# Kernel tuning notes

Measured on AMD Instinct MI355X. Metric: run time of the kernel, lower is better.

Reference implementation:

```python
import jax, jax.numpy as jnp
import numpy as np

PAD = 0

def setup_inputs() -> dict:
    key = jax.random.key(0)
    k1, k2, k3, k4 = jax.random.split(key, 4)
    B, S, F, V, H, D = 64, 256, 4, 50257, 768, 512
    words = jax.random.randint(k1, (B, S, F), 0, V, dtype=jnp.int64)  # pad_index=0 occurs rarely at random
    E = jax.random.normal(k2, (V, H), dtype=jnp.float32) * 0.02      # stand-in for transformer last_hidden_state producer
    W = jax.random.normal(k3, (H, D), dtype=jnp.float32) * 0.02      # FFN projection weight
    b = jax.random.normal(k4, (D,), dtype=jnp.float32) * 0.02
    return {"words": words, "E": E, "W": W, "b": b}

def reference(words, E, W, b):
    # words: [B, S, F] subword ids; mask out pad subwords
    mask = (words != PAD)                                  # [B,S,F] bool
    sub = E[words] * mask[..., None].astype(E.dtype)       # [B,S,F,H], pads zeroed
    cnt = mask.sum(-1).astype(E.dtype)                     # [B,S] subwords per word
    # segment-mean over the fix_len axis; fully-padded words -> 0 (matches pad_sequence(..., 0))
    word_emb = sub.sum(-2) / jnp.maximum(cnt, 1.0)[..., None]   # [B,S,H]
    word_emb = jnp.where((cnt > 0)[..., None], word_emb, 0.0)
    return word_emb @ W + b                                # [B,S,D]
```

## Files before the change

### kernel.cpp

```cpp
#include <hip/hip_runtime.h>
#include <hip/hip_bf16.h>

#define M_TOT 16384
#define K_TOT 768
#define N_TOT 512

typedef __attribute__((ext_vector_type(8))) __bf16 bf16x8;
typedef __attribute__((ext_vector_type(4))) float f32x4;

static __device__ __forceinline__ ushort f2bf(float x) {
  union { float f; unsigned int u; } v; v.f = x;
  unsigned int r = v.u + 0x7fffu + ((v.u >> 16) & 1u);
  return (ushort)(r >> 16);
}

static __device__ __forceinline__ void load_lds16(const ushort* g, ushort* l) {
  __builtin_amdgcn_global_load_lds(
      (const __attribute__((address_space(1))) void*)g,
      (__attribute__((address_space(3))) void*)l, 16, 0, 0);
}

__global__ __launch_bounds__(256) void prep_kernel(
    const int* __restrict__ words, const float* __restrict__ E,
    const float* __restrict__ W, ushort* __restrict__ A,
    ushort* __restrict__ Wt) {
  const int bid = blockIdx.x;
  const int t = threadIdx.x;
  if (bid < M_TOT / 4) {
    const int row  = bid * 4 + (t >> 6);
    const int lane = t & 63;
    const int4 w4 = *reinterpret_cast<const int4*>(words + (size_t)row * 4);
    const int ids[4] = {w4.x, w4.y, w4.z, w4.w};

    float a[12];
#pragma unroll
    for (int i = 0; i < 12; ++i) a[i] = 0.f;
    float cnt = 0.f;

#pragma unroll
    for (int f = 0; f < 4; ++f) {
      const int id = ids[f];
      if (id != 0) {
        const float4* __restrict__ src =
            reinterpret_cast<const float4*>(E + (size_t)id * K_TOT);
#pragma unroll
        for (int c = 0; c < 3; ++c) {
          const float4 v = src[c * 64 + lane];
          a[c * 4 + 0] += v.x; a[c * 4 + 1] += v.y;
          a[c * 4 + 2] += v.z; a[c * 4 + 3] += v.w;
        }
        cnt += 1.f;
      }
    }
    const float s = (cnt > 0.f) ? (1.f / cnt) : 0.f;
    ushort* dst = A + (size_t)row * K_TOT;
#pragma unroll
    for (int c = 0; c < 3; ++c) {
      ushort4 o;
      o.x = f2bf(a[c * 4 + 0] * s);
      o.y = f2bf(a[c * 4 + 1] * s);
      o.z = f2bf(a[c * 4 + 2] * s);
      o.w = f2bf(a[c * 4 + 3] * s);
      *reinterpret_cast<ushort4*>(dst + c * 256 + lane * 4) = o;
    }
  } else {
    __shared__ float tile[64][65];
    const int b2 = bid - M_TOT / 4;
    const int k0 = (b2 % (K_TOT / 64)) * 64;
    const int n0 = (b2 / (K_TOT / 64)) * 64;
#pragma unroll
    for (int i = 0; i < 4; ++i) {
      const int idx = t + i * 256;
      const int r = idx >> 4;
      const int c = (idx & 15) * 4;
      const float4 v = *reinterpret_cast<const float4*>(
          W + (size_t)(k0 + r) * N_TOT + n0 + c);
      tile[r][c + 0] = v.x; tile[r][c + 1] = v.y;
      tile[r][c + 2] = v.z; tile[r][c + 3] = v.w;
    }
    __syncthreads();
#pragma unroll
    for (int i = 0; i < 4; ++i) {
      const int idx = t + i * 256;
      const int rn = idx >> 4;
      const int ck = (idx & 15) * 4;
      ushort4 o;
      o.x = f2bf(tile[ck + 0][rn]);
      o.y = f2bf(tile[ck + 1][rn]);
      o.z = f2bf(tile[ck + 2][rn]);
      o.w = f2bf(tile[ck + 3][rn]);
      *reinterpret_cast<ushort4*>(Wt + (size_t)(n0 + rn) * K_TOT + k0 + ck) = o;
    }
  }
}

__global__ __launch_bounds__(256) void gemm_kernel(
    const ushort* __restrict__ A, const ushort* __restrict__ Bt,
    const float* __restrict__ bias, float* __restrict__ out) {
  __shared__ ushort Al[128 * 64];
  __shared__ ushort Bl[128 * 64];
  const int t    = threadIdx.x;
  const int lane = t & 63;
  const int w    = t >> 6;
  const int bm   = blockIdx.x >> 2;
  const int bn   = blockIdx.x & 3;
  const int wr   = w >> 1;
  const int wc   = w & 1;

  f32x4 acc[4][4];
#pragma unroll
  for (int m = 0; m < 4; ++m)
#pragma unroll
    for (int n = 0; n < 4; ++n) acc[m][n] = (f32x4){0.f, 0.f, 0.f, 0.f};

  const int srow = t >> 3;
  const int sseg = t & 7;
  const ushort* aptr = A  + (size_t)(bm * 128 + srow) * K_TOT + sseg * 8;
  const ushort* bptr = Bt + (size_t)(bn * 128 + srow) * K_TOT + sseg * 8;

  for (int kt = 0; kt < K_TOT / 64; ++kt) {
    __syncthreads();
#pragma unroll
    for (int i = 0; i < 4; ++i) {
      load_lds16(aptr + (size_t)i * 32 * K_TOT + kt * 64,
                 &Al[(i * 256 + w * 64) * 8]);
      load_lds16(bptr + (size_t)i * 32 * K_TOT + kt * 64,
                 &Bl[(i * 256 + w * 64) * 8]);
    }
    __syncthreads();

#pragma unroll
    for (int kk = 0; kk < 2; ++kk) {
      bf16x8 af[4], bf_[4];
      const int ks = kk * 4 + (lane >> 4);
#pragma unroll
      for (int m = 0; m < 4; ++m)
        af[m] = *reinterpret_cast<const bf16x8*>(
            &Al[(wr * 64 + m * 16 + (lane & 15)) * 64 + ks * 8]);
#pragma unroll
      for (int n = 0; n < 4; ++n)
        bf_[n] = *reinterpret_cast<const bf16x8*>(
            &Bl[(wc * 64 + n * 16 + (lane & 15)) * 64 + ks * 8]);
#pragma unroll
      for (int m = 0; m < 4; ++m)
#pragma unroll
        for (int n = 0; n < 4; ++n)
          acc[m][n] = __builtin_amdgcn_mfma_f32_16x16x32_bf16(
              af[m], bf_[n], acc[m][n], 0, 0, 0);
    }
  }

  const int colBase = bn * 128 + wc * 64 + (lane & 15);
  const int rowBase = bm * 128 + wr * 64 + ((lane >> 4) << 2);
#pragma unroll
  for (int n = 0; n < 4; ++n) {
    const float bv = bias[colBase + n * 16];
#pragma unroll
    for (int m = 0; m < 4; ++m) {
#pragma unroll
      for (int j = 0; j < 4; ++j) {
        out[(size_t)(rowBase + m * 16 + j) * N_TOT + colBase + n * 16] =
            acc[m][n][j] + bv;
      }
    }
  }
}

extern "C" void kernel_launch(void* const* d_in, const int* in_sizes, int n_in,
                              void* d_out, int out_size, void* d_ws,
                              size_t ws_size, hipStream_t stream) {
  const int*   words = (const int*)d_in[0];
  const float* E     = (const float*)d_in[1];
  const float* W     = (const float*)d_in[2];
  const float* b     = (const float*)d_in[3];
  float* out = (float*)d_out;

  ushort* Aws  = (ushort*)d_ws;
  ushort* Wtws = Aws + (size_t)M_TOT * K_TOT;

  hipLaunchKernelGGL(prep_kernel,
                     dim3(M_TOT / 4 + (K_TOT / 64) * (N_TOT / 64)), dim3(256),
                     0, stream, words, E, W, Aws, Wtws);
  hipLaunchKernelGGL(gemm_kernel, dim3((M_TOT / 128) * (N_TOT / 128)),
                     dim3(256), 0, stream, Aws, Wtws, b, out);
}
```

Baseline: 62.49 us.

## Double-buffer GEMM LDS tiles, branchless gather masking, nontemporal output stores

```diff
diff --git a/kernel.cpp b/kernel.cpp
--- a/kernel.cpp
+++ b/kernel.cpp
@@ -40,16 +40,15 @@
 #pragma unroll
     for (int f = 0; f < 4; ++f) {
       const int id = ids[f];
-      if (id != 0) {
-        const float4* __restrict__ src =
-            reinterpret_cast<const float4*>(E + (size_t)id * K_TOT);
-#pragma unroll
-        for (int c = 0; c < 3; ++c) {
-          const float4 v = src[c * 64 + lane];
-          a[c * 4 + 0] += v.x; a[c * 4 + 1] += v.y;
-          a[c * 4 + 2] += v.z; a[c * 4 + 3] += v.w;
-        }
-        cnt += 1.f;
+      const float msk = (id != 0) ? 1.f : 0.f;
+      cnt += msk;
+      const float4* __restrict__ src =
+          reinterpret_cast<const float4*>(E + (size_t)id * K_TOT);
+#pragma unroll
+      for (int c = 0; c < 3; ++c) {
+        const float4 v = src[c * 64 + lane];
+        a[c * 4 + 0] += v.x * msk; a[c * 4 + 1] += v.y * msk;
+        a[c * 4 + 2] += v.z * msk; a[c * 4 + 3] += v.w * msk;
       }
     }
     const float s = (cnt > 0.f) ? (1.f / cnt) : 0.f;
@@ -97,8 +96,8 @@
 __global__ __launch_bounds__(256) void gemm_kernel(
     const ushort* __restrict__ A, const ushort* __restrict__ Bt,
     const float* __restrict__ bias, float* __restrict__ out) {
-  __shared__ ushort Al[128 * 64];
-  __shared__ ushort Bl[128 * 64];
+  __shared__ ushort Al[2][128 * 64];
+  __shared__ ushort Bl[2][128 * 64];
   const int t    = threadIdx.x;
   const int lane = t & 63;
   const int w    = t >> 6;
@@ -118,37 +117,52 @@
   const ushort* aptr = A  + (size_t)(bm * 128 + srow) * K_TOT + sseg * 8;
   const ushort* bptr = Bt + (size_t)(bn * 128 + srow) * K_TOT + sseg * 8;
 
-  for (int kt = 0; kt < K_TOT / 64; ++kt) {
-    __syncthreads();
-#pragma unroll
-    for (int i = 0; i < 4; ++i) {
-      load_lds16(aptr + (size_t)i * 32 * K_TOT + kt * 64,
-                 &Al[(i * 256 + w * 64) * 8]);
-      load_lds16(bptr + (size_t)i * 32 * K_TOT + kt * 64,
-                 &Bl[(i * 256 + w * 64) * 8]);
-    }
-    __syncthreads();
-
+#define STAGE(buf, kt)                                                       \
+  do {                                                                       \
+    _Pragma("unroll") for (int i = 0; i < 4; ++i) {                          \
+      load_lds16(aptr + (size_t)i * 32 * K_TOT + (kt) * 64,                  \
+                 &Al[buf][(i * 256 + w * 64) * 8]);                          \
+      load_lds16(bptr + (size_t)i * 32 * K_TOT + (kt) * 64,                  \
+                 &Bl[buf][(i * 256 + w * 64) * 8]);                          \
+    }                                                                        \
+  } while (0)
+
+  STAGE(0, 0);
+  __syncthreads();
+
+  int cur = 0;
+  const int NT = K_TOT / 64;
+  for (int kt = 0; kt < NT; ++kt) {
+    if (kt + 1 < NT) {
+      if (cur == 0) STAGE(1, kt + 1); else STAGE(0, kt + 1);
+    }
 #pragma unroll
     for (int kk = 0; kk < 2; ++kk) {
       bf16x8 af[4], bf_[4];
       const int ks = kk * 4 + (lane >> 4);
+      const ushort* Ab = cur ? Al[1] : Al[0];
+      const ushort* Bb = cur ? Bl[1] : Bl[0];
 #pragma unroll
       for (int m = 0; m < 4; ++m)
         af[m] = *reinterpret_cast<const bf16x8*>(
-            &Al[(wr * 64 + m * 16 + (lane & 15)) * 64 + ks * 8]);
+            &Ab[(wr * 64 + m * 16 + (lane & 15)) * 64 + ks * 8]);
 #pragma unroll
       for (int n = 0; n < 4; ++n)
         bf_[n] = *reinterpret_cast<const bf16x8*>(
-            &Bl[(wc * 64 + n * 16 + (lane & 15)) * 64 + ks * 8]);
+            &Bb[(wc * 64 + n * 16 + (lane & 15)) * 64 + ks * 8]);
+      __builtin_amdgcn_s_setprio(1);
 #pragma unroll
       for (int m = 0; m < 4; ++m)
 #pragma unroll
         for (int n = 0; n < 4; ++n)
           acc[m][n] = __builtin_amdgcn_mfma_f32_16x16x32_bf16(
               af[m], bf_[n], acc[m][n], 0, 0, 0);
-    }
+      __builtin_amdgcn_s_setprio(0);
+    }
+    __syncthreads();
+    cur ^= 1;
   }
+#undef STAGE
 
   const int colBase = bn * 128 + wc * 64 + (lane & 15);
   const int rowBase = bm * 128 + wr * 64 + ((lane >> 4) << 2);
@@ -159,8 +173,9 @@
     for (int m = 0; m < 4; ++m) {
 #pragma unroll
       for (int j = 0; j < 4; ++j) {
-        out[(size_t)(rowBase + m * 16 + j) * N_TOT + colBase + n * 16] =
-            acc[m][n][j] + bv;
+        __builtin_nontemporal_store(
+            acc[m][n][j] + bv,
+            &out[(size_t)(rowBase + m * 16 + j) * N_TOT + colBase + n * 16]);
       }
     }
   }
```

Measured after the change: 61.21 us. 2.0% less time.
